# Kernel tuning notes

Measured on AMD Instinct MI355X. Metric: run time of the kernel, lower is better.

The kernel has to match this reference:

```python
import jax, jax.numpy as jnp
import numpy as np


def setup_inputs() -> dict:
    key = jax.random.key(0)
    k1, k2, k3, k4 = jax.random.split(key, 4)
    B, To, Tw, D = 64, 36, 32, 512  # Bo == Bw == B required by .diag()
    o = jax.random.normal(k1, (B, To, D), dtype=jnp.float32)
    u = jax.random.normal(k2, (B, To, D), dtype=jnp.float32)
    w = jax.random.normal(k3, (B, Tw, D), dtype=jnp.float32)
    mask = jax.random.randint(k4, (B, Tw), 0, 2).astype(jnp.int32)  # 1 = masked
    return {"o": o, "u": u, "w": w, "mask": mask}


def reference(o, u, w, mask):
    # o: (Bo, To, D) contextualized object feats; u: (Bo, To, D) uncontextualized;
    # w: (Bw, Tw, D) caption word feats; mask: (Bw, Tw) with 1 = padded word.
    D = w.shape[-1]
    # Original computes sum(Kw * Ku, 4) over a broadcast (Bw,Bo,Tw,To,D) tensor;
    # that is exactly a cross-batch contraction -> einsum.
    scores = jnp.einsum('wtd,bod->wbto', w, u) / jnp.sqrt(jnp.asarray(D, jnp.float32))
    att = jax.nn.softmax(scores, axis=3)              # softmax over objects To
    att_V_o = jnp.einsum('wbto,bod->wbtd', att, o)    # attention-weighted objects
    logits = jnp.einsum('wbtd,wtd->wbt', att_V_o, w)  # (Bw, Bo, Tw)
    log_sm = jax.nn.log_softmax(logits, axis=1)       # InfoNCE over Bo
    keep = 1.0 - mask.astype(log_sm.dtype)            # (Bw, Tw), 1 = valid word
    log_sm = log_sm * keep[:, None, :]
    num_non_mask = jnp.sum(keep, axis=1)[:, None, None]  # (Bw, 1, 1)
    log_sm = log_sm / (num_non_mask + 1e-6)
    loss_mat = jnp.sum(log_sm, axis=2)                # (Bw, Bo)
    loss = -jnp.mean(jnp.diagonal(loss_mat))
    return (loss, att, att_V_o)
```

## Files before the change

kernel.cpp:

```cpp
#include <hip/hip_runtime.h>

#define BB 64
#define TO 36
#define TW 32
#define DD 512

typedef short short8 __attribute__((ext_vector_type(8)));
typedef float floatx4 __attribute__((ext_vector_type(4)));


__device__ __forceinline__ unsigned short f2bf(float f) {
  unsigned int x = __builtin_bit_cast(unsigned int, f);
  x += 0x7FFFu + ((x >> 16) & 1u);
  return (unsigned short)(x >> 16);
}

__device__ __forceinline__ short8 ld8(const unsigned short* p) {
  return __builtin_bit_cast(short8, *(const uint4*)p);
}

__global__ __launch_bounds__(256) void prep_kernel(
    const float* __restrict__ o_g, const float* __restrict__ u_g,
    const float* __restrict__ w_g, unsigned short* __restrict__ wbf,
    unsigned short* __restrict__ ubf, unsigned short* __restrict__ ot) {
  const int blk = blockIdx.x, tid = threadIdx.x;
  if (blk < 512) {
    int i8 = blk * 256 + tid;
    const float4* src = (const float4*)w_g;
    float4 f0 = src[i8 * 2], f1 = src[i8 * 2 + 1];
    uint4 d;
    d.x = (unsigned)f2bf(f0.x) | ((unsigned)f2bf(f0.y) << 16);
    d.y = (unsigned)f2bf(f0.z) | ((unsigned)f2bf(f0.w) << 16);
    d.z = (unsigned)f2bf(f1.x) | ((unsigned)f2bf(f1.y) << 16);
    d.w = (unsigned)f2bf(f1.z) | ((unsigned)f2bf(f1.w) << 16);
    ((uint4*)wbf)[i8] = d;
  } else if (blk < 1088) {
    int i8 = (blk - 512) * 256 + tid;
    const float4* src = (const float4*)u_g;
    float4 f0 = src[i8 * 2], f1 = src[i8 * 2 + 1];
    uint4 d;
    d.x = (unsigned)f2bf(f0.x) | ((unsigned)f2bf(f0.y) << 16);
    d.y = (unsigned)f2bf(f0.z) | ((unsigned)f2bf(f0.w) << 16);
    d.z = (unsigned)f2bf(f1.x) | ((unsigned)f2bf(f1.y) << 16);
    d.w = (unsigned)f2bf(f1.z) | ((unsigned)f2bf(f1.w) << 16);
    ((uint4*)ubf)[i8] = d;
  } else {
    int t2 = (blk - 1088) * 256 + tid;
    int b = t2 >> 9, d = t2 & 511;
    uint4 bufv[8];
    unsigned short* buf = (unsigned short*)bufv;
#pragma unroll
    for (int o = 0; o < 64; ++o)
      buf[o] = (o < TO) ? f2bf(o_g[((b * TO + o) << 9) + d]) : (unsigned short)0;
    uint4* dst = (uint4*)(ot + ((size_t)((b << 9) + d) << 6));
#pragma unroll
    for (int i = 0; i < 8; ++i) dst[i] = bufv[i];
  }
}

__global__ __launch_bounds__(64) void main_kernel(
    const float* __restrict__ w_g,
    const unsigned short* __restrict__ wbf,
    const unsigned short* __restrict__ ubf,
    const unsigned short* __restrict__ ot,
    float* __restrict__ logits_ws,
    float* __restrict__ att_out,
    float* __restrict__ attV_out) {
  const int b = blockIdx.x, wb = blockIdx.y;
  const int lane = threadIdx.x;
  const int c = lane & 15;
  const int q = lane >> 4;

  __shared__ unsigned short att_s[TW][72];
  {
    unsigned int* p = (unsigned int*)&att_s[0][0];
#pragma unroll
    for (int i = 0; i < 18; ++i) p[lane + 64 * i] = 0u;
  }

  const unsigned short* wbp = wbf + (size_t)wb * TW * DD;
  const unsigned short* ubp = ubf + (size_t)b * TO * DD;

  floatx4 acc[2][3];
#pragma unroll
  for (int i = 0; i < 2; ++i)
#pragma unroll
    for (int j = 0; j < 3; ++j) acc[i][j] = (floatx4){0.f, 0.f, 0.f, 0.f};

  int r2 = 32 + c; if (r2 > 35) r2 = 35;
#pragma unroll 2
  for (int kk = 0; kk < 16; ++kk) {
    int k0 = kk * 32 + q * 8;
    short8 a0 = ld8(wbp + c * DD + k0);
    short8 a1 = ld8(wbp + (16 + c) * DD + k0);
    short8 u0 = ld8(ubp + c * DD + k0);
    short8 u1 = ld8(ubp + (16 + c) * DD + k0);
    short8 u2 = ld8(ubp + r2 * DD + k0);
    acc[0][0] = __builtin_amdgcn_mfma_f32_16x16x32_bf16(a0, u0, acc[0][0], 0, 0, 0);
    acc[0][1] = __builtin_amdgcn_mfma_f32_16x16x32_bf16(a0, u1, acc[0][1], 0, 0, 0);
    acc[0][2] = __builtin_amdgcn_mfma_f32_16x16x32_bf16(a0, u2, acc[0][2], 0, 0, 0);
    acc[1][0] = __builtin_amdgcn_mfma_f32_16x16x32_bf16(a1, u0, acc[1][0], 0, 0, 0);
    acc[1][1] = __builtin_amdgcn_mfma_f32_16x16x32_bf16(a1, u1, acc[1][1], 0, 0, 0);
    acc[1][2] = __builtin_amdgcn_mfma_f32_16x16x32_bf16(a1, u2, acc[1][2], 0, 0, 0);
  }

  const float scale = 0.04419417382415922f;
  float attv[2][3][4];
  const bool v2 = (c < 4);
#pragma unroll
  for (int mt = 0; mt < 2; ++mt) {
#pragma unroll
    for (int reg = 0; reg < 4; ++reg) {
      float s0 = acc[mt][0][reg] * scale;
      float s1 = acc[mt][1][reg] * scale;
      float s2 = acc[mt][2][reg] * scale;
      float m = fmaxf(s0, s1);
      if (v2) m = fmaxf(m, s2);
#pragma unroll
      for (int off = 1; off < 16; off <<= 1) m = fmaxf(m, __shfl_xor(m, off));
      float e0 = __expf(s0 - m);
      float e1 = __expf(s1 - m);
      float e2 = v2 ? __expf(s2 - m) : 0.f;
      float sum = e0 + e1 + e2;
#pragma unroll
      for (int off = 1; off < 16; off <<= 1) sum += __shfl_xor(sum, off);
      float inv = 1.f / sum;
      attv[mt][0][reg] = e0 * inv;
      attv[mt][1][reg] = e1 * inv;
      attv[mt][2][reg] = e2 * inv;
    }
  }

  float* attb = att_out + (size_t)(wb * BB + b) * TW * TO;
#pragma unroll
  for (int mt = 0; mt < 2; ++mt)
#pragma unroll
    for (int reg = 0; reg < 4; ++reg) {
      int t = mt * 16 + q * 4 + reg;
#pragma unroll
      for (int nt = 0; nt < 3; ++nt) {
        int oo = nt * 16 + c;
        if (oo < TO) {
          attb[t * TO + oo] = attv[mt][nt][reg];
          att_s[t][oo] = f2bf(attv[mt][nt][reg]);
        }
      }
    }
  __syncthreads();

  short8 a2[2][2];
#pragma unroll
  for (int mt = 0; mt < 2; ++mt)
#pragma unroll
    for (int kk = 0; kk < 2; ++kk)
      a2[mt][kk] = ld8(&att_s[mt * 16 + c][kk * 32 + q * 8]);

  const unsigned short* otp = ot + (size_t)b * DD * 64;
  const float* wrow = w_g + (size_t)wb * TW * DD;
  float* avb = attV_out + (size_t)(wb * BB + b) * TW * DD;
  float lp[2][4] = {{0.f, 0.f, 0.f, 0.f}, {0.f, 0.f, 0.f, 0.f}};

#pragma unroll 2
  for (int nt2 = 0; nt2 < 32; ++nt2) {
    int d0 = nt2 * 16;
    short8 b0 = ld8(otp + (d0 + c) * 64 + q * 8);
    short8 b1 = ld8(otp + (d0 + c) * 64 + 32 + q * 8);
#pragma unroll
    for (int mt = 0; mt < 2; ++mt) {
      floatx4 a = (floatx4){0.f, 0.f, 0.f, 0.f};
      a = __builtin_amdgcn_mfma_f32_16x16x32_bf16(a2[mt][0], b0, a, 0, 0, 0);
      a = __builtin_amdgcn_mfma_f32_16x16x32_bf16(a2[mt][1], b1, a, 0, 0, 0);
#pragma unroll
      for (int reg = 0; reg < 4; ++reg) {
        int t = mt * 16 + q * 4 + reg;
        float v = a[reg];
        avb[t * DD + d0 + c] = v;
        lp[mt][reg] = fmaf(v, wrow[t * DD + d0 + c], lp[mt][reg]);
      }
    }
  }

#pragma unroll
  for (int mt = 0; mt < 2; ++mt)
#pragma unroll
    for (int reg = 0; reg < 4; ++reg) {
      float s = lp[mt][reg];
#pragma unroll
      for (int off = 1; off < 16; off <<= 1) s += __shfl_xor(s, off);
      if (c == 0) {
        int t = mt * 16 + q * 4 + reg;
        logits_ws[(size_t)(wb * BB + b) * TW + t] = s;
      }
    }
}

__global__ __launch_bounds__(64) void loss_kernel(
    const float* __restrict__ logits, const int* __restrict__ mask,
    float* __restrict__ out) {
  int wb = blockIdx.x, lane = threadIdx.x;
  const float* lrow = logits + ((size_t)wb * BB + lane) * TW;
  float accv = 0.f, nnm = 0.f;
  for (int t = 0; t < TW; ++t) {
    float v = lrow[t];
    float m = v;
#pragma unroll
    for (int off = 1; off < 64; off <<= 1) m = fmaxf(m, __shfl_xor(m, off));
    float e = __expf(v - m);
    float s = e;
#pragma unroll
    for (int off = 1; off < 64; off <<= 1) s += __shfl_xor(s, off);
    float diag = __shfl(v, wb);
    float lsm = diag - m - __logf(s);
    float keep = 1.f - (float)mask[wb * TW + t];
    accv += lsm * keep;
    nnm += keep;
  }
  if (lane == 0) atomicAdd(out, -(accv / (nnm + 1e-6f)) * (1.f / 64.f));
}

extern "C" void kernel_launch(void* const* d_in, const int* in_sizes, int n_in,
                              void* d_out, int out_size, void* d_ws, size_t ws_size,
                              hipStream_t stream) {
  const float* o_g = (const float*)d_in[0];
  const float* u_g = (const float*)d_in[1];
  const float* w_g = (const float*)d_in[2];
  const int* mask  = (const int*)d_in[3];

  float* out = (float*)d_out;
  float* att_out  = out + 1;
  float* attV_out = out + 1 + (size_t)BB * BB * TW * TO;

  char* ws = (char*)d_ws;
  unsigned short* wbf = (unsigned short*)(ws + 0);
  unsigned short* ubf = (unsigned short*)(ws + 2097152);
  unsigned short* ot  = (unsigned short*)(ws + 4456448);
  float* logits       = (float*)(ws + 8650752);

  hipMemsetAsync(d_out, 0, sizeof(float), stream);
  prep_kernel<<<1216, 256, 0, stream>>>(o_g, u_g, w_g, wbf, ubf, ot);
  main_kernel<<<dim3(BB, BB), 64, 0, stream>>>(w_g, wbf, ubf, ot, logits,
                                               att_out, attV_out);
  loss_kernel<<<BB, 64, 0, stream>>>(logits, mask, out);
}
```

Baseline: 469.9 us.

## Transpose attV MFMA output for float4 stores and pack four word-batches per block

```diff
diff --git a/kernel.cpp b/kernel.cpp
--- a/kernel.cpp
+++ b/kernel.cpp
@@ -58,7 +58,7 @@
   }
 }
 
-__global__ __launch_bounds__(64) void main_kernel(
+__global__ __launch_bounds__(256) void main_kernel(
     const float* __restrict__ w_g,
     const unsigned short* __restrict__ wbf,
     const unsigned short* __restrict__ ubf,
@@ -66,14 +66,16 @@
     float* __restrict__ logits_ws,
     float* __restrict__ att_out,
     float* __restrict__ attV_out) {
-  const int b = blockIdx.x, wb = blockIdx.y;
-  const int lane = threadIdx.x;
+  const int b = blockIdx.x;
+  const int wv = threadIdx.x >> 6;
+  const int wb = blockIdx.y * 4 + wv;
+  const int lane = threadIdx.x & 63;
   const int c = lane & 15;
   const int q = lane >> 4;
 
-  __shared__ unsigned short att_s[TW][72];
+  __shared__ unsigned short att_s[4][TW][72];
   {
-    unsigned int* p = (unsigned int*)&att_s[0][0];
+    unsigned int* p = (unsigned int*)&att_s[wv][0][0];
 #pragma unroll
     for (int i = 0; i < 18; ++i) p[lane + 64 * i] = 0u;
   }
@@ -142,7 +144,7 @@
         int oo = nt * 16 + c;
         if (oo < TO) {
           attb[t * TO + oo] = attv[mt][nt][reg];
-          att_s[t][oo] = f2bf(attv[mt][nt][reg]);
+          att_s[wv][t][oo] = f2bf(attv[mt][nt][reg]);
         }
       }
     }
@@ -153,45 +155,71 @@
   for (int mt = 0; mt < 2; ++mt)
 #pragma unroll
     for (int kk = 0; kk < 2; ++kk)
-      a2[mt][kk] = ld8(&att_s[mt * 16 + c][kk * 32 + q * 8]);
+      a2[mt][kk] = ld8(&att_s[wv][mt * 16 + c][kk * 32 + q * 8]);
 
   const unsigned short* otp = ot + (size_t)b * DD * 64;
   const float* wrow = w_g + (size_t)wb * TW * DD;
   float* avb = attV_out + (size_t)(wb * BB + b) * TW * DD;
-  float lp[2][4] = {{0.f, 0.f, 0.f, 0.f}, {0.f, 0.f, 0.f, 0.f}};
-
-#pragma unroll 2
-  for (int nt2 = 0; nt2 < 32; ++nt2) {
-    int d0 = nt2 * 16;
+  float lp[2] = {0.f, 0.f};
+  float prevA3[2];
+
+  {
+    short8 b0 = ld8(otp + c * 64 + q * 8);
+    short8 b1 = ld8(otp + c * 64 + 32 + q * 8);
+#pragma unroll
+    for (int mt = 0; mt < 2; ++mt) {
+      floatx4 a = (floatx4){0.f, 0.f, 0.f, 0.f};
+      a = __builtin_amdgcn_mfma_f32_16x16x32_bf16(b0, a2[mt][0], a, 0, 0, 0);
+      a = __builtin_amdgcn_mfma_f32_16x16x32_bf16(b1, a2[mt][1], a, 0, 0, 0);
+      const int t = mt * 16 + c;
+      const int dd = q * 4;
+      float4 w4 = *(const float4*)&wrow[t * DD + dd];
+      lp[mt] += a[0] * w4.x + a[1] * w4.y + a[2] * w4.z + a[3] * w4.w;
+      float up = __shfl_up(a[3], 16);
+      if (q == 0) {
+        avb[t * DD + 0] = a[0];
+        avb[t * DD + 1] = a[1];
+        avb[t * DD + 2] = a[2];
+      } else {
+        float4 st = {up, a[0], a[1], a[2]};
+        *(float4*)&avb[t * DD + dd - 1] = st;
+      }
+      prevA3[mt] = a[3];
+    }
+  }
+
+#pragma unroll 4
+  for (int nt2 = 1; nt2 < 32; ++nt2) {
+    const int d0 = nt2 * 16;
     short8 b0 = ld8(otp + (d0 + c) * 64 + q * 8);
     short8 b1 = ld8(otp + (d0 + c) * 64 + 32 + q * 8);
 #pragma unroll
     for (int mt = 0; mt < 2; ++mt) {
       floatx4 a = (floatx4){0.f, 0.f, 0.f, 0.f};
-      a = __builtin_amdgcn_mfma_f32_16x16x32_bf16(a2[mt][0], b0, a, 0, 0, 0);
-      a = __builtin_amdgcn_mfma_f32_16x16x32_bf16(a2[mt][1], b1, a, 0, 0, 0);
-#pragma unroll
-      for (int reg = 0; reg < 4; ++reg) {
-        int t = mt * 16 + q * 4 + reg;
-        float v = a[reg];
-        avb[t * DD + d0 + c] = v;
-        lp[mt][reg] = fmaf(v, wrow[t * DD + d0 + c], lp[mt][reg]);
-      }
-    }
-  }
-
-#pragma unroll
-  for (int mt = 0; mt < 2; ++mt)
-#pragma unroll
-    for (int reg = 0; reg < 4; ++reg) {
-      float s = lp[mt][reg];
-#pragma unroll
-      for (int off = 1; off < 16; off <<= 1) s += __shfl_xor(s, off);
-      if (c == 0) {
-        int t = mt * 16 + q * 4 + reg;
-        logits_ws[(size_t)(wb * BB + b) * TW + t] = s;
-      }
-    }
+      a = __builtin_amdgcn_mfma_f32_16x16x32_bf16(b0, a2[mt][0], a, 0, 0, 0);
+      a = __builtin_amdgcn_mfma_f32_16x16x32_bf16(b1, a2[mt][1], a, 0, 0, 0);
+      const int t = mt * 16 + c;
+      const int dd = d0 + q * 4;
+      float4 w4 = *(const float4*)&wrow[t * DD + dd];
+      lp[mt] += a[0] * w4.x + a[1] * w4.y + a[2] * w4.z + a[3] * w4.w;
+      float up = __shfl_up(a[3], 16);
+      float carry = __shfl(prevA3[mt], c | 48);
+      float first = (q == 0) ? carry : up;
+      float4 st = {first, a[0], a[1], a[2]};
+      *(float4*)&avb[t * DD + dd - 1] = st;
+      prevA3[mt] = a[3];
+    }
+  }
+
+#pragma unroll
+  for (int mt = 0; mt < 2; ++mt) {
+    if (q == 3) avb[(mt * 16 + c) * DD + 511] = prevA3[mt];
+    float s = lp[mt];
+    s += __shfl_xor(s, 16);
+    s += __shfl_xor(s, 32);
+    if (lane < 16)
+      logits_ws[(size_t)(wb * BB + b) * TW + mt * 16 + lane] = s;
+  }
 }
 
 __global__ __launch_bounds__(64) void loss_kernel(
@@ -238,7 +266,7 @@
 
   hipMemsetAsync(d_out, 0, sizeof(float), stream);
   prep_kernel<<<1216, 256, 0, stream>>>(o_g, u_g, w_g, wbf, ubf, ot);
-  main_kernel<<<dim3(BB, BB), 64, 0, stream>>>(w_g, wbf, ubf, ot, logits,
-                                               att_out, attV_out);
+  main_kernel<<<dim3(BB, BB / 4), 256, 0, stream>>>(w_g, wbf, ubf, ot, logits,
+                                                    att_out, attV_out);
   loss_kernel<<<BB, 64, 0, stream>>>(logits, mask, out);
 }
```

Measured after the change: 435.3 us. -7.4%, faster.
